# Optimization experiments

Hardware: AMD Instinct MI355X
Metric: run time of the kernel (lower is better)

## Reference

```python
import jax, jax.numpy as jnp
import numpy as np

B, N, C = 16, 4096, 512
H = 8                      # num_heads
HEIGHT = WIDTH = 64        # input_resolution, HEIGHT*WIDTH == N
D = C // H                 # head_dim = 64
SCALE = D ** (-0.25)       # head_dim ** -0.25 (applied to both axial logits)


def setup_inputs() -> dict:
    key = jax.random.key(0)
    k0, k1, k2 = jax.random.split(key, 3)
    return {
        "x": jax.random.normal(k0, (B, N, C), jnp.float32),
        "W_qkv": jax.random.normal(k1, (C, 3 * C), jnp.float32) / np.sqrt(C).astype(np.float32),
        "b_qkv": jnp.zeros((3 * C,), jnp.float32),
        "W_proj": jax.random.normal(k2, (C, C), jnp.float32) / np.sqrt(C).astype(np.float32),
        "b_proj": jnp.zeros((C,), jnp.float32),
    }


def reference(x, W_qkv, b_qkv, W_proj, b_proj):
    Bx, Nx, Cx = x.shape
    # qkv projection -> [3, B, H, height, width, D]
    qkv = (x @ W_qkv + b_qkv).reshape(Bx, Nx, 3, H, D)
    qkv = jnp.transpose(qkv, (2, 0, 3, 1, 4)).reshape(3, Bx, H, HEIGHT, WIDTH, D)
    q, k, v = qkv[0], qkv[1], qkv[2]

    # row attention (channel_merge='concat'): contract over (width, channel)
    a = jnp.einsum('bhiwc,bhjwc->bhij', q, k) * SCALE          # [B,H,height,height]
    a = jax.nn.softmax(a, axis=-1)
    # column attention: contract over (height, channel)
    bm = jnp.einsum('bhtic,bhtjc->bhij', q, k) * SCALE         # [B,H,width,width]
    bm = jax.nn.softmax(bm, axis=-1)

    # coupled combination: (v_perm @ b^T) then a @ (...)
    # tmp[b,h,c,t,u] = sum_w v[b,h,t,w,c] * bm[b,h,u,w]
    tmp = jnp.einsum('bhtwc,bhuw->bhctu', v, bm)               # [B,H,D,height,width]
    out = jnp.einsum('bhij,bhcjw->bhciw', a, tmp)              # [B,H,D,height,width]

    out = out.reshape(Bx, Cx, Nx).transpose(0, 2, 1)           # [B,N,C]
    return out @ W_proj + b_proj
```

## Files before the change

### kernel.cpp

```cpp
#include <hip/hip_runtime.h>
#include <math.h>

#define SCALE_F 0.35355339059327373f

typedef unsigned short u16;
typedef unsigned int   u32;
typedef _Float16 f16;
typedef _Float16 f16x8 __attribute__((ext_vector_type(8)));
typedef float    f32x4 __attribute__((ext_vector_type(4)));

__device__ __forceinline__ u16 f2h(float f) { f16 h = (f16)f; return *(u16*)&h; }
__device__ __forceinline__ float h2f(u16 b) { f16 h = *(f16*)&b; return (float)h; }

__device__ __forceinline__ void glds16(const u16* g, char* l) {
    __builtin_amdgcn_global_load_lds((const __attribute__((address_space(1))) void*)g,
                                     (__attribute__((address_space(3))) void*)l, 16, 0, 0);
}
__device__ __forceinline__ f32x4 mfma16(f16x8 a, f16x8 b, f32x4 c) {
    return __builtin_amdgcn_mfma_f32_16x16x32_f16(a, b, c, 0, 0, 0);
}

__global__ __launch_bounds__(256) void to_f16(
    const float* __restrict__ X, u16* __restrict__ out)
{
    size_t i = ((size_t)blockIdx.x * 256 + threadIdx.x) * 8;
    float4 a = *(const float4*)(X + i);
    float4 b = *(const float4*)(X + i + 4);
    ushort4 r0, r1;
    r0.x = f2h(a.x); r0.y = f2h(a.y); r0.z = f2h(a.z); r0.w = f2h(a.w);
    r1.x = f2h(b.x); r1.y = f2h(b.y); r1.z = f2h(b.z); r1.w = f2h(b.w);
    *(ushort4*)(out + i)     = r0;
    *(ushort4*)(out + i + 4) = r1;
}

__global__ __launch_bounds__(256) void transpose_f16(
    const float* __restrict__ in, u16* __restrict__ out, int R, int C)
{
    __shared__ __align__(16) u16 T[64 * 80];
    const int c0 = blockIdx.x * 64, r0 = blockIdx.y * 64, z = blockIdx.z;
    const int t = threadIdx.x;
    const int rl = t >> 4, c4 = (t & 15) * 4;
    const float* base = in + (size_t)z * R * C;

    #pragma unroll
    for (int rr = 0; rr < 4; ++rr) {
        int r = rr * 16 + rl;
        float4 v = *(const float4*)(base + (size_t)(r0 + r) * C + c0 + c4);
        T[(c4 + 0) * 80 + r] = f2h(v.x);
        T[(c4 + 1) * 80 + r] = f2h(v.y);
        T[(c4 + 2) * 80 + r] = f2h(v.z);
        T[(c4 + 3) * 80 + r] = f2h(v.w);
    }
    __syncthreads();
    #pragma unroll
    for (int rep = 0; rep < 2; ++rep) {
        int idx = rep * 256 + t;
        int cl = idx >> 3, r8 = (idx & 7) * 8;
        *(float4*)(out + ((size_t)z * C + c0 + cl) * R + r0 + r8) =
            *(const float4*)&T[cl * 80 + r8];
    }
}

__global__ __launch_bounds__(256) void transpose16(
    const u16* __restrict__ in, u16* __restrict__ out)
{
    __shared__ __align__(16) u16 T[64 * 80];
    const int c0 = blockIdx.x * 64, r0 = blockIdx.y * 64, z = blockIdx.z;
    const int t = threadIdx.x;
    const int rl = t >> 3;
    const int c8 = (t & 7) * 8;
    const u16* base = in + (size_t)z * 512 * 4096;

    #pragma unroll
    for (int rr = 0; rr < 2; ++rr) {
        int r = rr * 32 + rl;
        const u16* p = base + (size_t)(r0 + r) * 4096 + c0 + c8;
        ushort4 v0 = *(const ushort4*)(p);
        ushort4 v1 = *(const ushort4*)(p + 4);
        T[(c8 + 0) * 80 + r] = v0.x;
        T[(c8 + 1) * 80 + r] = v0.y;
        T[(c8 + 2) * 80 + r] = v0.z;
        T[(c8 + 3) * 80 + r] = v0.w;
        T[(c8 + 4) * 80 + r] = v1.x;
        T[(c8 + 5) * 80 + r] = v1.y;
        T[(c8 + 6) * 80 + r] = v1.z;
        T[(c8 + 7) * 80 + r] = v1.w;
    }
    __syncthreads();
    #pragma unroll
    for (int rep = 0; rep < 2; ++rep) {
        int idx = rep * 256 + t;
        int cl = idx >> 3, r8 = (idx & 7) * 8;
        *(float4*)(out + ((size_t)z * 4096 + c0 + cl) * 512 + r0 + r8) =
            *(const float4*)&T[cl * 80 + r8];
    }
}

__global__ __launch_bounds__(512) void qkv_mfma(
    const u16* __restrict__ Xh, const u16* __restrict__ WT,
    const float* __restrict__ bias,
    u16* __restrict__ Q, u16* __restrict__ Kk, u16* __restrict__ Vt)
{
    __shared__ __align__(16) char smem[65536];

    const int id  = blockIdx.x;
    const int xcd = id & 7;
    const int jj  = id >> 3;
    const int mt  = xcd * 32 + jj / 6;
    const int nt  = jj % 6;

    const int t = threadIdx.x;
    const int wave = t >> 6, lane = t & 63;
    const int wm = wave & 1, wn = wave >> 1;
    const int quad = lane >> 4, l16 = lane & 15;
    const int m0 = mt * 256;

    const int srow = (wave & 3) * 64 + lane;
    size_t xoff[2], woff[2];
    int lb[2];
    #pragma unroll
    for (int p = 0; p < 2; ++p) {
        const int oct = p * 2 + (wave >> 2);
        xoff[p] = (size_t)(m0 + srow) * 512 + oct * 8;
        woff[p] = (size_t)(nt * 256 + srow) * 512 + oct * 8;
        lb[p]   = (p * 512 + wave * 64) * 16;
    }

    f32x4 acc[8][4];
    #pragma unroll
    for (int i = 0; i < 8; ++i)
        #pragma unroll
        for (int j = 0; j < 4; ++j) acc[i][j] = (f32x4){0.f, 0.f, 0.f, 0.f};

    #pragma unroll
    for (int p = 0; p < 2; ++p) {
        glds16(Xh + xoff[p], smem + lb[p]);
        glds16(WT + woff[p], smem + 16384 + lb[p]);
    }
    __syncthreads();

    for (int k0 = 0; k0 < 512; k0 += 32) {
        const int co = (k0 & 32) << 10;
        const int cn = co ^ 32768;
        char* Ac = smem + co;
        char* Bc = smem + co + 16384;
        if (k0 < 480) {
            #pragma unroll
            for (int p = 0; p < 2; ++p) {
                glds16(Xh + xoff[p] + k0 + 32, smem + cn + lb[p]);
                glds16(WT + woff[p] + k0 + 32, smem + cn + 16384 + lb[p]);
            }
        }

        f16x8 af[8], bf[4];
        #pragma unroll
        for (int i = 0; i < 8; ++i)
            af[i] = *(const f16x8*)(Ac + (quad * 256 + wm * 128 + i * 16 + l16) * 16);
        #pragma unroll
        for (int j = 0; j < 4; ++j)
            bf[j] = *(const f16x8*)(Bc + (quad * 256 + wn * 64 + j * 16 + l16) * 16);
        #pragma unroll
        for (int i = 0; i < 8; ++i)
            #pragma unroll
            for (int j = 0; j < 4; ++j)
                acc[i][j] = mfma16(af[i], bf[j], acc[i][j]);

        __syncthreads();
    }

    const int b   = m0 >> 12;
    const int nn0 = m0 & 4095;
    float bv[4];
    #pragma unroll
    for (int j = 0; j < 4; ++j) bv[j] = bias[nt * 256 + wn * 64 + j * 16 + l16];

    if (nt < 4) {
        u16* dst = (nt < 2) ? Q : Kk;
        const int hh = (nt & 1) * 4 + wn;
        char* Tw = smem + wave * 8192;
        u16* dsth = dst + ((size_t)(b * 8 + hh) * 4096 + nn0 + wm * 128) * 64;
        const int r8 = lane >> 3, l8 = lane & 7;
        #pragma unroll
        for (int g = 0; g < 2; ++g) {
            #pragma unroll
            for (int i2 = 0; i2 < 4; ++i2) {
                const int i = g * 4 + i2;
                #pragma unroll
                for (int j = 0; j < 4; ++j) {
                    #pragma unroll
                    for (int r = 0; r < 4; ++r) {
                        const int rl = i2 * 16 + quad * 4 + r;
                        const int cb = (j * 16 + l16) * 2;
                        *(u16*)(Tw + rl * 128 + (cb ^ ((rl & 7) << 4))) =
                            f2h(acc[i][j][r] + bv[j]);
                    }
                }
            }
            #pragma unroll
            for (int rep = 0; rep < 8; ++rep) {
                const int rl = rep * 8 + r8;
                f16x8 v = *(const f16x8*)(Tw + rl * 128 + ((l8 * 16) ^ ((rl & 7) << 4)));
                *(float4*)(dsth + (size_t)(g * 64 + rl) * 64 + l8 * 8) = *(float4*)&v;
            }
        }
    } else {
        u16* Trt = (u16*)smem;
        const int hb = (nt - 4) * 4;
        #pragma unroll
        for (int g = 0; g < 4; ++g) {
            __syncthreads();
            if (wn == g) {
                #pragma unroll
                for (int i = 0; i < 8; ++i)
                    #pragma unroll
                    for (int j = 0; j < 4; ++j)
                        #pragma unroll
                        for (int r = 0; r < 4; ++r)
                            Trt[(j * 16 + l16) * 272 + wm * 128 + i * 16 + quad * 4 + r] =
                                f2h(acc[i][j][r] + bv[j]);
            }
            __syncthreads();
            const int h = hb + g;
            u16* dstv = Vt + ((size_t)(b * 8 + h) * 64) * 4096 + nn0;
            #pragma unroll
            for (int rep = 0; rep < 4; ++rep) {
                int idx = rep * 512 + t;
                int d = idx >> 5, r8v = (idx & 31) * 8;
                *(float4*)(dstv + (size_t)d * 4096 + r8v) =
                    *(const float4*)&Trt[d * 272 + r8v];
            }
        }
    }
}

__global__ __launch_bounds__(256) void attn_logits(
    const u16* __restrict__ Q, const u16* __restrict__ Kk,
    float* __restrict__ Aout, float* __restrict__ Bmout)
{
    __shared__ float sm[64 * 68];
    __shared__ float red[128];

    const int bh   = blockIdx.x;
    const int mode = blockIdx.y;
    const int t    = threadIdx.x;
    const int wave = t >> 6, lane = t & 63;
    const int wr = wave & 1, wc = wave >> 1;
    const int quad = lane >> 4, l16 = lane & 15;

    const u16* Qb = Q  + (size_t)bh * 262144;
    const u16* Kb = Kk + (size_t)bh * 262144;

    const int rA0 = wr * 32 + l16, rA1 = rA0 + 16;
    const int rB0 = wc * 32 + l16, rB1 = rB0 + 16;

    f32x4 acc[2][2];
    #pragma unroll
    for (int i = 0; i < 2; ++i)
        #pragma unroll
        for (int j = 0; j < 2; ++j) acc[i][j] = (f32x4){0.f, 0.f, 0.f, 0.f};

    if (mode == 0) {
        const u16* pA0 = Qb + (size_t)rA0 * 4096;
        const u16* pA1 = Qb + (size_t)rA1 * 4096;
        const u16* pB0 = Kb + (size_t)rB0 * 4096;
        const u16* pB1 = Kb + (size_t)rB1 * 4096;
        #pragma unroll 4
        for (int k0 = 0; k0 < 4096; k0 += 32) {
            const int kk = k0 + quad * 8;
            f16x8 a0 = *(const f16x8*)(pA0 + kk);
            f16x8 a1 = *(const f16x8*)(pA1 + kk);
            f16x8 b0 = *(const f16x8*)(pB0 + kk);
            f16x8 b1 = *(const f16x8*)(pB1 + kk);
            acc[0][0] = mfma16(a0, b0, acc[0][0]);
            acc[0][1] = mfma16(a0, b1, acc[0][1]);
            acc[1][0] = mfma16(a1, b0, acc[1][0]);
            acc[1][1] = mfma16(a1, b1, acc[1][1]);
        }
    } else {
        #pragma unroll 4
        for (int k0 = 0; k0 < 4096; k0 += 32) {
            const int kk = k0 + quad * 8;
            const size_t base = (size_t)(kk >> 6) * 4096 + (kk & 63);
            f16x8 a0 = *(const f16x8*)(Qb + base + rA0 * 64);
            f16x8 a1 = *(const f16x8*)(Qb + base + rA1 * 64);
            f16x8 b0 = *(const f16x8*)(Kb + base + rB0 * 64);
            f16x8 b1 = *(const f16x8*)(Kb + base + rB1 * 64);
            acc[0][0] = mfma16(a0, b0, acc[0][0]);
            acc[0][1] = mfma16(a0, b1, acc[0][1]);
            acc[1][0] = mfma16(a1, b0, acc[1][0]);
            acc[1][1] = mfma16(a1, b1, acc[1][1]);
        }
    }

    #pragma unroll
    for (int i = 0; i < 2; ++i)
        #pragma unroll
        for (int j = 0; j < 2; ++j)
            #pragma unroll
            for (int r = 0; r < 4; ++r)
                sm[(wr * 32 + i * 16 + quad * 4 + r) * 68 + wc * 32 + j * 16 + l16] =
                    acc[i][j][r] * SCALE_F;
    __syncthreads();
    if (t < 64) {
        float m = -1e30f;
        for (int j = 0; j < 64; ++j) m = fmaxf(m, sm[t * 68 + j]);
        float ssum = 0.f;
        for (int j = 0; j < 64; ++j) ssum += __expf(sm[t * 68 + j] - m);
        red[t] = m;
        red[64 + t] = 1.0f / ssum;
    }
    __syncthreads();
    float* Out = ((mode == 0) ? Aout : Bmout) + (size_t)bh * 4096;
    #pragma unroll
    for (int rep = 0; rep < 16; ++rep) {
        int idx = rep * 256 + t;
        int i = idx >> 6, j = idx & 63;
        Out[idx] = __expf(sm[i * 68 + j] - red[i]) * red[64 + i];
    }
}

__global__ __launch_bounds__(256) void coupling(
    const u16* __restrict__ Vt, const float* __restrict__ Aatt,
    const float* __restrict__ Bm, u16* __restrict__ Yh)
{
    __shared__ __align__(16) u16 Ah[64 * 72];
    __shared__ __align__(16) u16 Bh[64 * 72];
    __shared__ __align__(16) u16 Tt[2][64 * 72];
    __shared__ __align__(16) u16 Ot[64 * 72];

    const int bh = blockIdx.x, cg = blockIdx.y;
    const int t = threadIdx.x;
    const int wave = t >> 6, lane = t & 63;
    const int wr = wave & 1, wc = wave >> 1;
    const int quad = lane >> 4, l16 = lane & 15;

    const float* Ab = Aatt + (size_t)bh * 4096;
    const float* Bb = Bm   + (size_t)bh * 4096;
    const u16*  Vb  = Vt   + (size_t)bh * 262144;
    u16* Yb = Yh + (size_t)bh * 262144;

    {
        const int row = t >> 2;
        const int colb = (t & 3) * 16;
        #pragma unroll
        for (int q = 0; q < 4; ++q) {
            float4 va = *(const float4*)(Ab + (size_t)row * 64 + colb + q * 4);
            Ah[row * 72 + colb + q * 4 + 0] = f2h(va.x);
            Ah[row * 72 + colb + q * 4 + 1] = f2h(va.y);
            Ah[row * 72 + colb + q * 4 + 2] = f2h(va.z);
            Ah[row * 72 + colb + q * 4 + 3] = f2h(va.w);
            float4 vb = *(const float4*)(Bb + (size_t)row * 64 + colb + q * 4);
            Bh[row * 72 + colb + q * 4 + 0] = f2h(vb.x);
            Bh[row * 72 + colb + q * 4 + 1] = f2h(vb.y);
            Bh[row * 72 + colb + q * 4 + 2] = f2h(vb.z);
            Bh[row * 72 + colb + q * 4 + 3] = f2h(vb.w);
        }
    }
    __syncthreads();

    for (int ci = 0; ci < 16; ++ci) {
        const int c = cg * 16 + ci;
        u16* tb = &Tt[ci & 1][0];

        f32x4 acc1[2][2];
        #pragma unroll
        for (int i = 0; i < 2; ++i)
            #pragma unroll
            for (int j = 0; j < 2; ++j) acc1[i][j] = (f32x4){0.f, 0.f, 0.f, 0.f};
        #pragma unroll
        for (int s = 0; s < 2; ++s) {
            f16x8 a1[2], b1[2];
            #pragma unroll
            for (int i = 0; i < 2; ++i)
                a1[i] = *(const f16x8*)&Bh[(wr * 32 + i * 16 + l16) * 72 + s * 32 + quad * 8];
            #pragma unroll
            for (int j = 0; j < 2; ++j)
                b1[j] = *(const f16x8*)(Vb + (size_t)c * 4096 +
                                        (size_t)(wc * 32 + j * 16 + l16) * 64 + s * 32 + quad * 8);
            #pragma unroll
            for (int i = 0; i < 2; ++i)
                #pragma unroll
                for (int j = 0; j < 2; ++j)
                    acc1[i][j] = mfma16(a1[i], b1[j], acc1[i][j]);
        }
        #pragma unroll
        for (int i = 0; i < 2; ++i)
            #pragma unroll
            for (int j = 0; j < 2; ++j)
                #pragma unroll
                for (int r = 0; r < 4; ++r)
                    tb[(wr * 32 + i * 16 + quad * 4 + r) * 72 + wc * 32 + j * 16 + l16] =
                        f2h(acc1[i][j][r]);
        __syncthreads();

        f32x4 acc2[2][2];
        #pragma unroll
        for (int i = 0; i < 2; ++i)
            #pragma unroll
            for (int j = 0; j < 2; ++j) acc2[i][j] = (f32x4){0.f, 0.f, 0.f, 0.f};
        #pragma unroll
        for (int s = 0; s < 2; ++s) {
            f16x8 a2[2], b2[2];
            #pragma unroll
            for (int i = 0; i < 2; ++i)
                a2[i] = *(const f16x8*)&Ah[(wr * 32 + i * 16 + l16) * 72 + s * 32 + quad * 8];
            #pragma unroll
            for (int u = 0; u < 2; ++u)
                b2[u] = *(const f16x8*)&tb[(wc * 32 + u * 16 + l16) * 72 + s * 32 + quad * 8];
            #pragma unroll
            for (int i = 0; i < 2; ++i)
                #pragma unroll
                for (int u = 0; u < 2; ++u)
                    acc2[i][u] = mfma16(a2[i], b2[u], acc2[i][u]);
        }
        #pragma unroll
        for (int i = 0; i < 2; ++i)
            #pragma unroll
            for (int u = 0; u < 2; ++u)
                #pragma unroll
                for (int r = 0; r < 4; ++r)
                    Ot[(wr * 32 + i * 16 + quad * 4 + r) * 72 + wc * 32 + u * 16 + l16] =
                        f2h(acc2[i][u][r]);
        __syncthreads();
        {
            const int row0 = t >> 3, l8 = t & 7;
            #pragma unroll
            for (int pass = 0; pass < 2; ++pass) {
                const int row = pass * 32 + row0;
                *(float4*)(Yb + (size_t)c * 4096 + row * 64 + l8 * 8) =
                    *(const float4*)&Ot[row * 72 + l8 * 8];
            }
        }
    }
}

__global__ __launch_bounds__(256) void proj_mfma(
    const u16* __restrict__ A, const u16* __restrict__ WT,
    const float* __restrict__ bias, float* __restrict__ Out)
{
    __shared__ __align__(16) char smem[32768];

    const int id  = blockIdx.x;
    const int xcd = id & 7;
    const int jj  = id >> 3;
    const int mt  = xcd * 64 + (jj >> 2);
    const int nt  = jj & 3;

    const int t = threadIdx.x;
    const int wave = t >> 6, lane = t & 63;
    const int wm = wave & 1, wn = wave >> 1;
    const int quad = lane >> 4, l16 = lane & 15;
    const int m0 = mt * 128;

    const int c0 = wave * 128 + lane;
    const int c1 = c0 + 64;
    const size_t aoff0 = (size_t)(m0 + (c0 & 127)) * 512 + (c0 >> 7) * 8;
    const size_t aoff1 = (size_t)(m0 + (c1 & 127)) * 512 + (c1 >> 7) * 8;
    const size_t woff0 = (size_t)(nt * 128 + (c0 & 127)) * 512 + (c0 >> 7) * 8;
    const size_t woff1 = (size_t)(nt * 128 + (c1 & 127)) * 512 + (c1 >> 7) * 8;
    const int lb0 = (wave * 128) * 16;
    const int lb1 = lb0 + 64 * 16;

    f32x4 acc[4][4];
    #pragma unroll
    for (int i = 0; i < 4; ++i)
        #pragma unroll
        for (int j = 0; j < 4; ++j) acc[i][j] = (f32x4){0.f, 0.f, 0.f, 0.f};

    glds16(A  + aoff0, smem + lb0);
    glds16(A  + aoff1, smem + lb1);
    glds16(WT + woff0, smem + 8192 + lb0);
    glds16(WT + woff1, smem + 8192 + lb1);
    __syncthreads();

    for (int k0 = 0; k0 < 512; k0 += 32) {
        const int co = (k0 & 32) << 9;
        const int cn = co ^ 16384;
        char* Ac = smem + co;
        char* Bc = smem + 8192 + co;
        if (k0 < 480) {
            glds16(A  + aoff0 + k0 + 32, smem + cn + lb0);
            glds16(A  + aoff1 + k0 + 32, smem + cn + lb1);
            glds16(WT + woff0 + k0 + 32, smem + 8192 + cn + lb0);
            glds16(WT + woff1 + k0 + 32, smem + 8192 + cn + lb1);
        }

        f16x8 af[4], bf[4];
        #pragma unroll
        for (int i = 0; i < 4; ++i)
            af[i] = *(const f16x8*)(Ac + (quad * 128 + wm * 64 + i * 16 + l16) * 16);
        #pragma unroll
        for (int j = 0; j < 4; ++j)
            bf[j] = *(const f16x8*)(Bc + (quad * 128 + wn * 64 + j * 16 + l16) * 16);
        #pragma unroll
        for (int i = 0; i < 4; ++i)
            #pragma unroll
            for (int j = 0; j < 4; ++j)
                acc[i][j] = mfma16(af[i], bf[j], acc[i][j]);

        __syncthreads();
    }

    float bv[4];
    #pragma unroll
    for (int j = 0; j < 4; ++j) bv[j] = bias[nt * 128 + wn * 64 + j * 16 + l16];

    #pragma unroll
    for (int i = 0; i < 4; ++i) {
        const int rowb = m0 + wm * 64 + i * 16 + quad * 4;
        #pragma unroll
        for (int j = 0; j < 4; ++j) {
            const int col = nt * 128 + wn * 64 + j * 16 + l16;
            #pragma unroll
            for (int r = 0; r < 4; ++r)
                Out[(size_t)(rowb + r) * 512 + col] = acc[i][j][r] + bv[j];
        }
    }
}

extern "C" void kernel_launch(void* const* d_in, const int* in_sizes, int n_in,
                              void* d_out, int out_size, void* d_ws, size_t ws_size,
                              hipStream_t stream)
{
    const float* x     = (const float*)d_in[0];
    const float* Wqkv  = (const float*)d_in[1];
    const float* bqkv  = (const float*)d_in[2];
    const float* Wproj = (const float*)d_in[3];
    const float* bproj = (const float*)d_in[4];
    float* out = (float*)d_out;

    u16* Xh  = (u16*)d_ws;
    u16* Qh  = Xh + 33554432;
    u16* Kh  = Qh + 33554432;
    u16* Vth = Kh + 33554432;
    u16* WqT = Vth + 33554432;
    u16* WpT = WqT + 786432;
    float* Aa = (float*)(WpT + 262144);
    float* Bm = Aa + 524288;
    u16* Yh  = Xh;
    u16* Ytb = Kh;

    to_f16        <<<16384, 256, 0, stream>>>(x, Xh);
    transpose_f16 <<<dim3(24, 8, 1),  256, 0, stream>>>(Wqkv,  WqT, 512, 1536);
    transpose_f16 <<<dim3(8, 8, 1),   256, 0, stream>>>(Wproj, WpT, 512, 512);
    qkv_mfma      <<<1536,            512, 0, stream>>>(Xh, WqT, bqkv, Qh, Kh, Vth);
    attn_logits   <<<dim3(128, 2),    256, 0, stream>>>(Qh, Kh, Aa, Bm);
    coupling      <<<dim3(128, 4),    256, 0, stream>>>(Vth, Aa, Bm, Yh);
    transpose16   <<<dim3(64, 8, 16), 256, 0, stream>>>(Yh, Ytb);
    proj_mfma     <<<2048,            256, 0, stream>>>(Ytb, WpT, bproj, out);
}
```

Measured before the change: 648.5 us.

## Deepen GEMM LDS pipelines to four stages with vmcnt waits and MFMA priority

Replaces the double-buffered global-to-LDS loops in the QKV and output-projection GEMMs with a four-stage ring buffer. Loads are issued three tiles ahead, and each iteration waits on a partial vmcnt plus a raw s_barrier instead of a full __syncthreads. MFMA blocks are also wrapped in s_setprio to favour matrix issue. The aim is to hide global load latency better, at the cost of doubling LDS per block, which may reduce occupancy (128KB for qkv, 64KB for proj).

```diff
diff --git a/kernel.cpp b/kernel.cpp
--- a/kernel.cpp
+++ b/kernel.cpp
@@ -101,7 +101,7 @@
     const float* __restrict__ bias,
     u16* __restrict__ Q, u16* __restrict__ Kk, u16* __restrict__ Vt)
 {
-    __shared__ __align__(16) char smem[65536];
+    __shared__ __align__(16) char smem[131072];
 
     const int id  = blockIdx.x;
     const int xcd = id & 7;
@@ -132,41 +132,60 @@
         #pragma unroll
         for (int j = 0; j < 4; ++j) acc[i][j] = (f32x4){0.f, 0.f, 0.f, 0.f};
 
-    #pragma unroll
-    for (int p = 0; p < 2; ++p) {
-        glds16(Xh + xoff[p], smem + lb[p]);
-        glds16(WT + woff[p], smem + 16384 + lb[p]);
-    }
-    __syncthreads();
-
-    for (int k0 = 0; k0 < 512; k0 += 32) {
-        const int co = (k0 & 32) << 10;
-        const int cn = co ^ 32768;
-        char* Ac = smem + co;
-        char* Bc = smem + co + 16384;
-        if (k0 < 480) {
-            #pragma unroll
-            for (int p = 0; p < 2; ++p) {
-                glds16(Xh + xoff[p] + k0 + 32, smem + cn + lb[p]);
-                glds16(WT + woff[p] + k0 + 32, smem + cn + 16384 + lb[p]);
-            }
-        }
-
-        f16x8 af[8], bf[4];
-        #pragma unroll
-        for (int i = 0; i < 8; ++i)
-            af[i] = *(const f16x8*)(Ac + (quad * 256 + wm * 128 + i * 16 + l16) * 16);
-        #pragma unroll
-        for (int j = 0; j < 4; ++j)
-            bf[j] = *(const f16x8*)(Bc + (quad * 256 + wn * 64 + j * 16 + l16) * 16);
-        #pragma unroll
-        for (int i = 0; i < 8; ++i)
-            #pragma unroll
-            for (int j = 0; j < 4; ++j)
-                acc[i][j] = mfma16(af[i], bf[j], acc[i][j]);
-
-        __syncthreads();
-    }
+#define STAGE_QKV(T, S) do {                                                 \
+        char* _d = smem + (S) * 32768;                                       \
+        const int _k = (T) * 32;                                             \
+        glds16(Xh + xoff[0] + _k, _d + lb[0]);                               \
+        glds16(Xh + xoff[1] + _k, _d + lb[1]);                               \
+        glds16(WT + woff[0] + _k, _d + 16384 + lb[0]);                       \
+        glds16(WT + woff[1] + _k, _d + 16384 + lb[1]);                       \
+    } while (0)
+
+#define COMPUTE_QKV(S) do {                                                  \
+        char* _Ac = smem + (S) * 32768;                                      \
+        char* _Bc = _Ac + 16384;                                             \
+        f16x8 _af[8], _bf[4];                                                \
+        _Pragma("unroll")                                                    \
+        for (int _i = 0; _i < 8; ++_i)                                       \
+            _af[_i] = *(const f16x8*)(_Ac + (quad * 256 + wm * 128 + _i * 16 + l16) * 16); \
+        _Pragma("unroll")                                                    \
+        for (int _j = 0; _j < 4; ++_j)                                       \
+            _bf[_j] = *(const f16x8*)(_Bc + (quad * 256 + wn * 64 + _j * 16 + l16) * 16);  \
+        __builtin_amdgcn_s_setprio(1);                                       \
+        _Pragma("unroll")                                                    \
+        for (int _i = 0; _i < 8; ++_i)                                       \
+            _Pragma("unroll")                                                \
+            for (int _j = 0; _j < 4; ++_j)                                   \
+                acc[_i][_j] = mfma16(_af[_i], _bf[_j], acc[_i][_j]);         \
+        __builtin_amdgcn_s_setprio(0);                                       \
+    } while (0)
+
+    STAGE_QKV(0, 0);
+    STAGE_QKV(1, 1);
+    STAGE_QKV(2, 2);
+
+    for (int kt = 0; kt < 13; ++kt) {
+        asm volatile("s_waitcnt vmcnt(8)" ::: "memory");
+        __builtin_amdgcn_s_barrier();
+        __builtin_amdgcn_sched_barrier(0);
+        STAGE_QKV(kt + 3, (kt + 3) & 3);
+        COMPUTE_QKV(kt & 3);
+    }
+    asm volatile("s_waitcnt vmcnt(8)" ::: "memory");
+    __builtin_amdgcn_s_barrier();
+    __builtin_amdgcn_sched_barrier(0);
+    COMPUTE_QKV(1);
+    asm volatile("s_waitcnt vmcnt(4)" ::: "memory");
+    __builtin_amdgcn_s_barrier();
+    __builtin_amdgcn_sched_barrier(0);
+    COMPUTE_QKV(2);
+    asm volatile("s_waitcnt vmcnt(0)" ::: "memory");
+    __builtin_amdgcn_s_barrier();
+    __builtin_amdgcn_sched_barrier(0);
+    COMPUTE_QKV(3);
+
+#undef STAGE_QKV
+#undef COMPUTE_QKV
 
     const int b   = m0 >> 12;
     const int nn0 = m0 & 4095;
@@ -438,7 +457,7 @@
     const u16* __restrict__ A, const u16* __restrict__ WT,
     const float* __restrict__ bias, float* __restrict__ Out)
 {
-    __shared__ __align__(16) char smem[32768];
+    __shared__ __align__(16) char smem[65536];
 
     const int id  = blockIdx.x;
     const int xcd = id & 7;
@@ -467,39 +486,60 @@
         #pragma unroll
         for (int j = 0; j < 4; ++j) acc[i][j] = (f32x4){0.f, 0.f, 0.f, 0.f};
 
-    glds16(A  + aoff0, smem + lb0);
-    glds16(A  + aoff1, smem + lb1);
-    glds16(WT + woff0, smem + 8192 + lb0);
-    glds16(WT + woff1, smem + 8192 + lb1);
-    __syncthreads();
-
-    for (int k0 = 0; k0 < 512; k0 += 32) {
-        const int co = (k0 & 32) << 9;
-        const int cn = co ^ 16384;
-        char* Ac = smem + co;
-        char* Bc = smem + 8192 + co;
-        if (k0 < 480) {
-            glds16(A  + aoff0 + k0 + 32, smem + cn + lb0);
-            glds16(A  + aoff1 + k0 + 32, smem + cn + lb1);
-            glds16(WT + woff0 + k0 + 32, smem + 8192 + cn + lb0);
-            glds16(WT + woff1 + k0 + 32, smem + 8192 + cn + lb1);
-        }
-
-        f16x8 af[4], bf[4];
-        #pragma unroll
-        for (int i = 0; i < 4; ++i)
-            af[i] = *(const f16x8*)(Ac + (quad * 128 + wm * 64 + i * 16 + l16) * 16);
-        #pragma unroll
-        for (int j = 0; j < 4; ++j)
-            bf[j] = *(const f16x8*)(Bc + (quad * 128 + wn * 64 + j * 16 + l16) * 16);
-        #pragma unroll
-        for (int i = 0; i < 4; ++i)
-            #pragma unroll
-            for (int j = 0; j < 4; ++j)
-                acc[i][j] = mfma16(af[i], bf[j], acc[i][j]);
-
-        __syncthreads();
-    }
+#define STAGE_P(T, S) do {                                                   \
+        char* _d = smem + (S) * 16384;                                       \
+        const int _k = (T) * 32;                                             \
+        glds16(A  + aoff0 + _k, _d + lb0);                                   \
+        glds16(A  + aoff1 + _k, _d + lb1);                                   \
+        glds16(WT + woff0 + _k, _d + 8192 + lb0);                            \
+        glds16(WT + woff1 + _k, _d + 8192 + lb1);                            \
+    } while (0)
+
+#define COMPUTE_P(S) do {                                                    \
+        char* _Ac = smem + (S) * 16384;                                      \
+        char* _Bc = _Ac + 8192;                                              \
+        f16x8 _af[4], _bf[4];                                                \
+        _Pragma("unroll")                                                    \
+        for (int _i = 0; _i < 4; ++_i)                                       \
+            _af[_i] = *(const f16x8*)(_Ac + (quad * 128 + wm * 64 + _i * 16 + l16) * 16); \
+        _Pragma("unroll")                                                    \
+        for (int _j = 0; _j < 4; ++_j)                                       \
+            _bf[_j] = *(const f16x8*)(_Bc + (quad * 128 + wn * 64 + _j * 16 + l16) * 16); \
+        __builtin_amdgcn_s_setprio(1);                                       \
+        _Pragma("unroll")                                                    \
+        for (int _i = 0; _i < 4; ++_i)                                       \
+            _Pragma("unroll")                                                \
+            for (int _j = 0; _j < 4; ++_j)                                   \
+                acc[_i][_j] = mfma16(_af[_i], _bf[_j], acc[_i][_j]);         \
+        __builtin_amdgcn_s_setprio(0);                                       \
+    } while (0)
+
+    STAGE_P(0, 0);
+    STAGE_P(1, 1);
+    STAGE_P(2, 2);
+
+    for (int kt = 0; kt < 13; ++kt) {
+        asm volatile("s_waitcnt vmcnt(8)" ::: "memory");
+        __builtin_amdgcn_s_barrier();
+        __builtin_amdgcn_sched_barrier(0);
+        STAGE_P(kt + 3, (kt + 3) & 3);
+        COMPUTE_P(kt & 3);
+    }
+    asm volatile("s_waitcnt vmcnt(8)" ::: "memory");
+    __builtin_amdgcn_s_barrier();
+    __builtin_amdgcn_sched_barrier(0);
+    COMPUTE_P(1);
+    asm volatile("s_waitcnt vmcnt(4)" ::: "memory");
+    __builtin_amdgcn_s_barrier();
+    __builtin_amdgcn_sched_barrier(0);
+    COMPUTE_P(2);
+    asm volatile("s_waitcnt vmcnt(0)" ::: "memory");
+    __builtin_amdgcn_s_barrier();
+    __builtin_amdgcn_sched_barrier(0);
+    COMPUTE_P(3);
+
+#undef STAGE_P
+#undef COMPUTE_P
 
     float bv[4];
     #pragma unroll
```

Measured after the change: 641.9 us. No clear change (-1.0%).
